# Optimization experiments

Measured on AMD Instinct MI355X. Metric: run time of the kernel, lower is better.

## Reference

```python
import jax, jax.numpy as jnp
import numpy as np

B, C, H, I = 32, 8, 512, 512


def act(x):
    # CustomActivation == hardtanh: (|x+1| - |x-1|) / 2
    return (jnp.abs(x + 1.0) - jnp.abs(x - 1.0)) * 0.5


def setup_inputs() -> dict:
    key = jax.random.key(0)
    ks = jax.random.split(key, 12)
    inp = jax.random.normal(ks[0], (B, C, H, I), dtype=jnp.float32)
    p_mask = jax.random.normal(ks[1], (H, I), dtype=jnp.float32)
    # Wp: tril(randn) with diagonal filled to 1 (matches __init__ + the no_grad
    # tril/clamp projection in forward, which is a no-op right after init).
    Wp = jnp.tril(jax.random.normal(ks[2], (H, H), dtype=jnp.float32))
    Wp = Wp - jnp.diag(jnp.diag(Wp)) + jnp.eye(H, dtype=jnp.float32)
    Wp_diag = jnp.ones((H,), dtype=jnp.float32)
    Wzp = jax.random.normal(ks[3], (H, H), dtype=jnp.float32)
    s = 1.0 / np.sqrt(I)
    def lin(k):
        kw, kb = jax.random.split(k)
        W = jax.random.uniform(kw, (I, I), jnp.float32, -s, s)
        b = jax.random.uniform(kb, (I,), jnp.float32, -s, s)
        return W, b
    p_lin_w, p_lin_b = lin(ks[4])
    z_lin_w, z_lin_b = lin(ks[5])
    fc1_w, fc1_b = lin(ks[6])
    fc2_w, fc2_b = lin(ks[7])
    return {
        'input': inp, 'p_mask': p_mask, 'Wp': Wp, 'Wp_diag': Wp_diag, 'Wzp': Wzp,
        'p_lin_w': p_lin_w, 'p_lin_b': p_lin_b,
        'z_lin_w': z_lin_w, 'z_lin_b': z_lin_b,
        'fc1_w': fc1_w, 'fc1_b': fc1_b, 'fc2_w': fc2_w, 'fc2_b': fc2_b,
    }


def reference(input, p_mask, Wp, Wp_diag, Wzp,
              p_lin_w, p_lin_b, z_lin_w, z_lin_b,
              fc1_w, fc1_b, fc2_w, fc2_b):
    x = input * (1.0 / 5000.0)                      # [B,C,H,I]
    p_set = x * act(p_mask)                         # split_input, broadcast over B,C
    Wp_eff = Wp + jnp.diag(Wp_diag)                 # [H,H]
    # per-channel Wp @ p_set[c], batched over B and C in one GEMM
    tp = jnp.einsum('hk,bcki->bchi', Wp_eff, p_set)
    tp = act(act(tp) @ p_lin_w.T + p_lin_b)         # p_output_layer
    tz = jnp.einsum('hk,bchi->bchi', Wzp, tp)       # wait-free channel-batched GEMM
    tz = act(act(tz) @ z_lin_w.T + z_lin_b)         # z_output_layer
    # sum over in_channel (out_channel==1 so broadcast-accumulate == sum)
    combined = tp.sum(axis=1) + tz.sum(axis=1) + x[:, 0]  # [B,H,I]
    out = jax.nn.relu(combined @ fc1_w.T + fc1_b)
    out = out @ fc2_w.T + fc2_b
    return out
```

## Files before the change

kernel.cpp:

```cpp
#include <hip/hip_runtime.h>

namespace {

constexpr int Bn = 32, Cn = 8, Hn = 512, In = 512;
constexpr size_t HI = (size_t)Hn * In;
constexpr float SC = 1.0f / 5000.0f;

using s16x8 = __attribute__((ext_vector_type(8))) short;
using f32x4 = __attribute__((ext_vector_type(4))) float;

__device__ __forceinline__ float actf(float x) {
    return fminf(1.0f, fmaxf(-1.0f, x));
}

__device__ __forceinline__ unsigned short f2bf(float f) {
    unsigned u = __builtin_bit_cast(unsigned, f);
    u += 0x7FFFu + ((u >> 16) & 1u);
    return (unsigned short)(u >> 16);
}
__device__ __forceinline__ float bf2f(unsigned short h) {
    return __builtin_bit_cast(float, (unsigned)h << 16);
}

__device__ __forceinline__ void async16(const void* g, void* l) {
    __builtin_amdgcn_global_load_lds(
        (const __attribute__((address_space(1))) unsigned*)g,
        (__attribute__((address_space(3))) unsigned*)l, 16, 0, 0);
}

#define CFENCE asm volatile("" ::: "memory")

template<int EPI, bool PCOL, bool TRI>
__global__ __launch_bounds__(256, 3) void mfma_gemm(
    const unsigned short* __restrict__ A,
    const unsigned short* __restrict__ Bt,
    const float* __restrict__ bias,
    const float* __restrict__ zrow,
    unsigned short* __restrict__ out0,
    unsigned short* __restrict__ out1,
    float* __restrict__ outf,
    size_t sB, size_t sC)
{
    __shared__ __align__(16) char lds[2][16384];

    const int tid  = threadIdx.x;
    const int wid  = tid >> 6, lane = tid & 63;
    const int wr   = wid >> 1, wc = wid & 1;
    const int l15  = lane & 15, kq = lane >> 4;

    const int bid = blockIdx.x;
    const int p = ((bid >> 5) << 3) | (bid & 7);
    const int q = (bid >> 3) & 3;
    const int rt = PCOL ? q : p;
    const int ct = PCOL ? (p & 3) : q;
    const size_t zb = PCOL ? (size_t)(p >> 2) : 0;

    const char* Ab = (const char*)A + (size_t)rt * 131072;
    const char* Bb = (const char*)(Bt + zb * sB) + (size_t)ct * 131072;

    f32x4 acc[4][4] = {};

    const int o0  = tid * 16;
    const int r0s = o0 >> 6;
    const int c0s = o0 & 63;
    const int csw = c0s ^ (((r0s >> 1) & 3) << 4);

    auto stage = [&](char* buf, int k0b) {
        async16(Ab + (size_t)r0s * 1024 + k0b + csw,        buf + wid * 1024);
        async16(Ab + (size_t)(64 + r0s) * 1024 + k0b + csw, buf + 4096 + wid * 1024);
        async16(Bb + (size_t)r0s * 1024 + k0b + csw,        buf + 8192 + wid * 1024);
        async16(Bb + (size_t)(64 + r0s) * 1024 + k0b + csw, buf + 12288 + wid * 1024);
    };
    auto compute = [&](const char* buf) {
        s16x8 a[4], b[4];
        const int kx = kq * 16 ^ (((l15 >> 1) & 3) << 4);
        const int ar = wr * 64 + l15;
        const int br = wc * 64 + l15;
        #pragma unroll
        for (int m = 0; m < 4; ++m)
            a[m] = *(const s16x8*)(buf + (size_t)(ar + m * 16) * 64 + kx);
        #pragma unroll
        for (int n = 0; n < 4; ++n)
            b[n] = *(const s16x8*)(buf + 8192 + (size_t)(br + n * 16) * 64 + kx);
        #pragma unroll
        for (int m = 0; m < 4; ++m)
            #pragma unroll
            for (int n = 0; n < 4; ++n)
                acc[m][n] = __builtin_amdgcn_mfma_f32_16x16x32_bf16(a[m], b[n], acc[m][n], 0, 0, 0);
    };

    const int kSteps = TRI ? (rt + 1) * 4 : 16;

    stage(lds[0], 0);
    stage(lds[1], 64);

    #pragma unroll 1
    for (int ks = 0; ks < kSteps; ks += 2) {
        const bool more = (ks + 2 < kSteps);
        asm volatile("s_waitcnt vmcnt(4)" ::: "memory");
        __builtin_amdgcn_s_barrier(); CFENCE;
        compute(lds[0]);
        CFENCE; __builtin_amdgcn_s_barrier();
        if (more) stage(lds[0], (ks + 2) * 64);
        if (more) asm volatile("s_waitcnt vmcnt(4)" ::: "memory");
        else      asm volatile("s_waitcnt vmcnt(0)" ::: "memory");
        __builtin_amdgcn_s_barrier(); CFENCE;
        compute(lds[1]);
        CFENCE; __builtin_amdgcn_s_barrier();
        if (more) stage(lds[1], (ks + 3) * 64);
    }

    const int cb = ct * 128 + wc * 64 + l15;
    const int rb = rt * 128 + wr * 64 + (kq << 2);
    #pragma unroll
    for (int m = 0; m < 4; ++m) {
        #pragma unroll
        for (int n = 0; n < 4; ++n) {
            const int c = cb + n * 16;
            #pragma unroll
            for (int j = 0; j < 4; ++j) {
                const int r = rb + m * 16 + j;
                float v = acc[m][n][j];
                const size_t idx = zb * sC + (size_t)r * 512 + c;
                if (EPI == 0) {
                    out0[idx] = f2bf(actf(v));
                } else if (EPI == 1) {
                    float tp = actf(v + bias[c]);
                    out0[idx] = f2bf(tp);
                    out1[idx] = f2bf(actf(zrow[r & 511] * tp));
                } else if (EPI == 2) {
                    out0[idx] = f2bf(actf(v + bias[c]));
                } else if (EPI == 3) {
                    out0[idx] = f2bf(fmaxf(v + bias[c], 0.0f));
                } else {
                    outf[idx] = v + bias[c];
                }
            }
        }
    }
}

__global__ __launch_bounds__(256) void reduce_both(
    const unsigned short* __restrict__ tp,
    const unsigned short* __restrict__ tz,
    const float* __restrict__ x0,
    unsigned short* __restrict__ comb)
{
    size_t idx = (size_t)blockIdx.x * 256 + threadIdx.x;
    size_t b = idx >> 16;
    size_t p = (idx & 65535) * 4;
    float4 xv = *(const float4*)&x0[(b * Cn) * HI + p];
    float s0 = xv.x * SC, s1 = xv.y * SC, s2 = xv.z * SC, s3 = xv.w * SC;
    #pragma unroll
    for (int c = 0; c < Cn; ++c) {
        size_t q = (b * Cn + c) * HI + p;
        ushort4 a = *(const ushort4*)&tp[q];
        ushort4 d = *(const ushort4*)&tz[q];
        s0 += bf2f(a.x) + bf2f(d.x);
        s1 += bf2f(a.y) + bf2f(d.y);
        s2 += bf2f(a.z) + bf2f(d.z);
        s3 += bf2f(a.w) + bf2f(d.w);
    }
    ushort4 o;
    o.x = f2bf(s0); o.y = f2bf(s1); o.z = f2bf(s2); o.w = f2bf(s3);
    *(ushort4*)&comb[b * HI + p] = o;
}

__global__ __launch_bounds__(256) void transpose_mask(
    const float* __restrict__ x, const float* __restrict__ mask,
    unsigned short* __restrict__ xst)
{
    __shared__ float t[64][65];
    const int bc = blockIdx.z;
    const int i0 = blockIdx.x * 64, k0 = blockIdx.y * 64;
    const int r4 = threadIdx.x >> 6, cc = threadIdx.x & 63;
    const float* xp = x + (size_t)bc * HI;
    #pragma unroll
    for (int it = 0; it < 16; ++it) {
        int kl = it * 4 + r4;
        size_t g = (size_t)(k0 + kl) * In + i0 + cc;
        t[kl][cc] = xp[g] * (actf(mask[g]) * SC);
    }
    __syncthreads();
    unsigned short* op = xst + (size_t)bc * HI;
    #pragma unroll
    for (int it = 0; it < 16; ++it) {
        int il = it * 4 + r4;
        op[(size_t)(i0 + il) * Hn + k0 + cc] = f2bf(t[cc][il]);
    }
}

__global__ __launch_bounds__(256) void prep_wpe_bf(
    const float* __restrict__ Wp, const float* __restrict__ Wpd,
    unsigned short* __restrict__ o)
{
    int idx = blockIdx.x * 256 + threadIdx.x;
    int i = idx >> 9, j = idx & 511;
    o[idx] = f2bf(Wp[idx] + (i == j ? Wpd[i] : 0.0f));
}

__global__ __launch_bounds__(256) void conv_bf(
    const float* __restrict__ s, unsigned short* __restrict__ o)
{
    int idx = blockIdx.x * 256 + threadIdx.x;
    o[idx] = f2bf(s[idx]);
}

__global__ __launch_bounds__(64) void rowsum(
    const float* __restrict__ W, float* __restrict__ zr)
{
    int h = blockIdx.x, l = threadIdx.x;
    float s = 0.0f;
    for (int k = l; k < Hn; k += 64) s += W[h * Hn + k];
    #pragma unroll
    for (int off = 32; off; off >>= 1) s += __shfl_down(s, off, 64);
    if (!l) zr[h] = s;
}

}

extern "C" void kernel_launch(void* const* d_in, const int* in_sizes, int n_in,
                              void* d_out, int out_size, void* d_ws, size_t ws_size,
                              hipStream_t stream)
{
    const float* input  = (const float*)d_in[0];
    const float* p_mask = (const float*)d_in[1];
    const float* Wp     = (const float*)d_in[2];
    const float* Wpd    = (const float*)d_in[3];
    const float* Wzp    = (const float*)d_in[4];
    const float* plw    = (const float*)d_in[5];
    const float* plb    = (const float*)d_in[6];
    const float* zlw    = (const float*)d_in[7];
    const float* zlb    = (const float*)d_in[8];
    const float* f1w    = (const float*)d_in[9];
    const float* f1b    = (const float*)d_in[10];
    const float* f2w    = (const float*)d_in[11];
    const float* f2b    = (const float*)d_in[12];

    constexpr size_t WB = 512 * 512 * 2;
    char* w = (char*)d_ws;
    auto alloc = [&](size_t bytes) { char* p = w; w += (bytes + 255) & ~255ull; return p; };

    unsigned short* Wpeb  = (unsigned short*)alloc(WB);
    unsigned short* plwb  = (unsigned short*)alloc(WB);
    unsigned short* zlwb  = (unsigned short*)alloc(WB);
    unsigned short* f1wb  = (unsigned short*)alloc(WB);
    unsigned short* f2wb  = (unsigned short*)alloc(WB);
    float*          zrw   = (float*)alloc(512 * 4);
    unsigned short* combb = (unsigned short*)alloc((size_t)Bn * HI * 2);
    unsigned short* out1  = (unsigned short*)alloc((size_t)Bn * HI * 2);

    size_t fixedB = (size_t)(w - (char*)d_ws);
    int chunk = 32;
    while (chunk > 1 &&
           fixedB + 4ull * (size_t)chunk * Cn * HI * 2 + 4096 > ws_size)
        chunk >>= 1;
    const size_t CB = (size_t)chunk * Cn * HI * 2;
    unsigned short* xst   = (unsigned short*)alloc(CB);
    unsigned short* tpact = (unsigned short*)alloc(CB);
    unsigned short* tpb   = (unsigned short*)alloc(CB);
    unsigned short* tzin  = (unsigned short*)alloc(CB);
    unsigned short* tzb   = xst;

    prep_wpe_bf<<<512 * 512 / 256, 256, 0, stream>>>(Wp, Wpd, Wpeb);
    conv_bf<<<1024, 256, 0, stream>>>(plw, plwb);
    conv_bf<<<1024, 256, 0, stream>>>(zlw, zlwb);
    conv_bf<<<1024, 256, 0, stream>>>(f1w, f1wb);
    conv_bf<<<1024, 256, 0, stream>>>(f2w, f2wb);
    rowsum<<<512, 64, 0, stream>>>(Wzp, zrw);

    for (int b0 = 0; b0 < Bn; b0 += chunk) {
        const int nc = chunk * Cn;
        const float* inp_c = input + (size_t)b0 * Cn * HI;

        transpose_mask<<<dim3(8, 8, nc), 256, 0, stream>>>(inp_c, p_mask, xst);
        mfma_gemm<0, true, true><<<nc * 16, 256, 0, stream>>>(
            Wpeb, xst, nullptr, nullptr, tpact, nullptr, nullptr, HI, HI);
        mfma_gemm<1, false, false><<<nc * 16, 256, 0, stream>>>(
            tpact, plwb, plb, zrw, tpb, tzin, nullptr, 0, 0);
        mfma_gemm<2, false, false><<<nc * 16, 256, 0, stream>>>(
            tzin, zlwb, zlb, nullptr, tzb, nullptr, nullptr, 0, 0);
        reduce_both<<<chunk * 256, 256, 0, stream>>>(
            tpb, tzb, inp_c, combb + (size_t)b0 * HI);
    }

    mfma_gemm<3, false, false><<<512, 256, 0, stream>>>(
        combb, f1wb, f1b, nullptr, out1, nullptr, nullptr, 0, 0);
    mfma_gemm<4, false, false><<<512, 256, 0, stream>>>(
        out1, f2wb, f2b, nullptr, nullptr, nullptr, (float*)d_out, 0, 0);
}
```

Before: 555.9 us.

## Use 256x256 tiled 8-wave GEMM with interleaved prefetch for main chain

```diff
diff --git a/kernel.cpp b/kernel.cpp
--- a/kernel.cpp
+++ b/kernel.cpp
@@ -29,17 +29,167 @@
 }
 
 #define CFENCE asm volatile("" ::: "memory")
+#define BAR do { CFENCE; __builtin_amdgcn_s_barrier(); CFENCE; } while (0)
 
 template<int EPI, bool PCOL, bool TRI>
-__global__ __launch_bounds__(256, 3) void mfma_gemm(
+__global__ __launch_bounds__(512, 2) void gemm256_8p(
     const unsigned short* __restrict__ A,
     const unsigned short* __restrict__ Bt,
     const float* __restrict__ bias,
     const float* __restrict__ zrow,
     unsigned short* __restrict__ out0,
     unsigned short* __restrict__ out1,
-    float* __restrict__ outf,
     size_t sB, size_t sC)
+{
+    __shared__ __align__(16) char lds[131072];
+    char* daA = lds;
+    char* dbA = lds + 32768;
+    char* daB = lds + 65536;
+    char* dbB = lds + 98304;
+
+    const int tid = threadIdx.x;
+    const int lane = tid & 63, l15 = lane & 15, kq = lane >> 4;
+    const int wid = tid >> 6, wm = wid >> 2, wn = wid & 3;
+
+    const int bid = blockIdx.x;
+    int rt, ct; size_t zb;
+    if (PCOL) {
+        const int p = ((bid >> 5) << 3) | (bid & 7);
+        const int q = (bid >> 3) & 3;
+        zb = (size_t)p; rt = q >> 1; ct = q & 1;
+    } else {
+        const int p = ((bid >> 4) << 3) | (bid & 7);
+        const int q = (bid >> 3) & 1;
+        zb = 0; rt = p; ct = q;
+    }
+
+    const char* Ab = (const char*)A + (size_t)rt * 256 * 1024;
+    const char* Bb = (const char*)(Bt + zb * sB) + (size_t)ct * 256 * 1024;
+
+    const int nkt = TRI ? (rt + 1) * 4 : 8;
+    const int nit = nkt >> 1;
+
+    const int srow8 = tid >> 3;
+    const int csw   = ((tid & 7) ^ (srow8 & 7)) << 4;
+
+    auto stageH = [&](const char* src, int kt, int half, char* dstTile) {
+        const char* s = src + ((size_t)half * 128 + srow8) * 1024 + kt * 128 + csw;
+        char* d = dstTile + half * 16384 + tid * 16;
+        async16(s,             d);
+        async16(s + 64 * 1024, d + 8192);
+    };
+
+    const int kx0 = ((kq    ) ^ (l15 & 7)) << 4;
+    const int kx1 = ((kq + 4) ^ (l15 & 7)) << 4;
+
+    auto rdA4 = [&](const char* tile, int mlo, s16x8 a[2][4]) {
+        #pragma unroll
+        for (int i = 0; i < 4; ++i) {
+            const int row = wm * 128 + (mlo + i) * 16 + l15;
+            a[0][i] = *(const s16x8*)(tile + row * 128 + kx0);
+            a[1][i] = *(const s16x8*)(tile + row * 128 + kx1);
+        }
+    };
+    auto rdB2 = [&](const char* tile, int nlo, s16x8 b[2][2]) {
+        #pragma unroll
+        for (int j = 0; j < 2; ++j) {
+            const int row = wn * 64 + (nlo + j) * 16 + l15;
+            b[0][j] = *(const s16x8*)(tile + row * 128 + kx0);
+            b[1][j] = *(const s16x8*)(tile + row * 128 + kx1);
+        }
+    };
+
+    f32x4 acc[8][4] = {};
+
+    auto QMM = [&](s16x8 a[2][4], s16x8 b[2][2], int mlo, int nlo) {
+        __builtin_amdgcn_s_setprio(1);
+        #pragma unroll
+        for (int kk = 0; kk < 2; ++kk)
+            #pragma unroll
+            for (int i = 0; i < 4; ++i)
+                #pragma unroll
+                for (int j = 0; j < 2; ++j)
+                    acc[mlo + i][nlo + j] = __builtin_amdgcn_mfma_f32_16x16x32_bf16(
+                        a[kk][i], b[kk][j], acc[mlo + i][nlo + j], 0, 0, 0);
+        __builtin_amdgcn_s_setprio(0);
+    };
+
+    stageH(Bb, 0, 0, daB); stageH(Bb, 0, 1, daB);
+    stageH(Ab, 0, 0, daA); stageH(Ab, 0, 1, daA);
+    stageH(Bb, 1, 0, dbB); stageH(Bb, 1, 1, dbB);
+    asm volatile("s_waitcnt vmcnt(4)" ::: "memory");
+    BAR;
+
+    #pragma unroll 1
+    for (int t = 0; t < nit; ++t) {
+        const int j = 2 * t;
+        const bool more = (t + 1 < nit);
+        s16x8 a03[2][4], a47[2][4], b01[2][2], b23[2][2];
+
+        rdA4(daA, 0, a03); rdB2(daB, 0, b01);
+        stageH(Ab, j + 1, 0, dbA);
+        BAR; QMM(a03, b01, 0, 0); BAR;
+        rdB2(daB, 2, b23);
+        stageH(Ab, j + 1, 1, dbA);
+        BAR; QMM(a03, b23, 0, 2); BAR;
+        rdA4(daA, 4, a47);
+        if (more) stageH(Bb, j + 2, 0, daB);
+        BAR; QMM(a47, b23, 4, 2); BAR;
+        if (more) stageH(Bb, j + 2, 1, daB);
+        BAR; QMM(a47, b01, 4, 0);
+        if (more) asm volatile("s_waitcnt vmcnt(4)" ::: "memory");
+        else      asm volatile("s_waitcnt vmcnt(0)" ::: "memory");
+        BAR;
+
+        rdA4(dbA, 0, a03); rdB2(dbB, 0, b01);
+        if (more) stageH(Ab, j + 2, 0, daA);
+        BAR; QMM(a03, b01, 0, 0); BAR;
+        rdB2(dbB, 2, b23);
+        if (more) stageH(Ab, j + 2, 1, daA);
+        BAR; QMM(a03, b23, 0, 2); BAR;
+        rdA4(dbA, 4, a47);
+        if (more) stageH(Bb, j + 3, 0, dbB);
+        BAR; QMM(a47, b23, 4, 2); BAR;
+        if (more) stageH(Bb, j + 3, 1, dbB);
+        BAR; QMM(a47, b01, 4, 0);
+        if (more) { asm volatile("s_waitcnt vmcnt(4)" ::: "memory"); BAR; }
+        else BAR;
+    }
+
+    const int rbase = rt * 256 + wm * 128 + kq * 4;
+    const int cb    = ct * 256 + wn * 64 + l15;
+    #pragma unroll
+    for (int mi = 0; mi < 8; ++mi) {
+        #pragma unroll
+        for (int n = 0; n < 4; ++n) {
+            const int c = cb + n * 16;
+            const float bs = (EPI == 0) ? 0.0f : bias[c];
+            #pragma unroll
+            for (int jj = 0; jj < 4; ++jj) {
+                const size_t r = (size_t)rbase + mi * 16 + jj;
+                const size_t idx = zb * sC + r * 512 + c;
+                float v = acc[mi][n][jj];
+                if (EPI == 0) {
+                    out0[idx] = f2bf(actf(v));
+                } else if (EPI == 1) {
+                    float tp = actf(v + bs);
+                    out0[idx] = f2bf(tp);
+                    out1[idx] = f2bf(actf(zrow[r & 511] * tp));
+                } else {
+                    out0[idx] = f2bf(actf(v + bs));
+                }
+            }
+        }
+    }
+}
+
+template<int EPI>
+__global__ __launch_bounds__(256, 3) void mfma_gemm128(
+    const unsigned short* __restrict__ A,
+    const unsigned short* __restrict__ Bt,
+    const float* __restrict__ bias,
+    unsigned short* __restrict__ out0,
+    float* __restrict__ outf)
 {
     __shared__ __align__(16) char lds[2][16384];
 
@@ -51,12 +201,10 @@
     const int bid = blockIdx.x;
     const int p = ((bid >> 5) << 3) | (bid & 7);
     const int q = (bid >> 3) & 3;
-    const int rt = PCOL ? q : p;
-    const int ct = PCOL ? (p & 3) : q;
-    const size_t zb = PCOL ? (size_t)(p >> 2) : 0;
+    const int rt = p, ct = q;
 
     const char* Ab = (const char*)A + (size_t)rt * 131072;
-    const char* Bb = (const char*)(Bt + zb * sB) + (size_t)ct * 131072;
+    const char* Bb = (const char*)Bt + (size_t)ct * 131072;
 
     f32x4 acc[4][4] = {};
 
@@ -89,55 +237,41 @@
                 acc[m][n] = __builtin_amdgcn_mfma_f32_16x16x32_bf16(a[m], b[n], acc[m][n], 0, 0, 0);
     };
 
-    const int kSteps = TRI ? (rt + 1) * 4 : 16;
-
     stage(lds[0], 0);
     stage(lds[1], 64);
 
     #pragma unroll 1
-    for (int ks = 0; ks < kSteps; ks += 2) {
-        const bool more = (ks + 2 < kSteps);
+    for (int ks = 0; ks < 16; ks += 2) {
+        const bool more = (ks + 2 < 16);
         asm volatile("s_waitcnt vmcnt(4)" ::: "memory");
-        __builtin_amdgcn_s_barrier(); CFENCE;
+        BAR;
         compute(lds[0]);
-        CFENCE; __builtin_amdgcn_s_barrier();
+        BAR;
         if (more) stage(lds[0], (ks + 2) * 64);
         if (more) asm volatile("s_waitcnt vmcnt(4)" ::: "memory");
         else      asm volatile("s_waitcnt vmcnt(0)" ::: "memory");
-        __builtin_amdgcn_s_barrier(); CFENCE;
+        BAR;
         compute(lds[1]);
-        CFENCE; __builtin_amdgcn_s_barrier();
+        BAR;
         if (more) stage(lds[1], (ks + 3) * 64);
     }
 
     const int cb = ct * 128 + wc * 64 + l15;
     const int rb = rt * 128 + wr * 64 + (kq << 2);
     #pragma unroll
-    for (int m = 0; m < 4; ++m) {
+    for (int m = 0; m < 4; ++m)
         #pragma unroll
         for (int n = 0; n < 4; ++n) {
             const int c = cb + n * 16;
             #pragma unroll
             for (int j = 0; j < 4; ++j) {
                 const int r = rb + m * 16 + j;
-                float v = acc[m][n][j];
-                const size_t idx = zb * sC + (size_t)r * 512 + c;
-                if (EPI == 0) {
-                    out0[idx] = f2bf(actf(v));
-                } else if (EPI == 1) {
-                    float tp = actf(v + bias[c]);
-                    out0[idx] = f2bf(tp);
-                    out1[idx] = f2bf(actf(zrow[r & 511] * tp));
-                } else if (EPI == 2) {
-                    out0[idx] = f2bf(actf(v + bias[c]));
-                } else if (EPI == 3) {
-                    out0[idx] = f2bf(fmaxf(v + bias[c], 0.0f));
-                } else {
-                    outf[idx] = v + bias[c];
-                }
+                const size_t idx = (size_t)r * 512 + c;
+                float v = acc[m][n][j] + bias[c];
+                if (EPI == 3) out0[idx] = f2bf(fmaxf(v, 0.0f));
+                else          outf[idx] = v;
             }
         }
-    }
 }
 
 __global__ __launch_bounds__(256) void reduce_both(
@@ -274,18 +408,16 @@
         const float* inp_c = input + (size_t)b0 * Cn * HI;
 
         transpose_mask<<<dim3(8, 8, nc), 256, 0, stream>>>(inp_c, p_mask, xst);
-        mfma_gemm<0, true, true><<<nc * 16, 256, 0, stream>>>(
-            Wpeb, xst, nullptr, nullptr, tpact, nullptr, nullptr, HI, HI);
-        mfma_gemm<1, false, false><<<nc * 16, 256, 0, stream>>>(
-            tpact, plwb, plb, zrw, tpb, tzin, nullptr, 0, 0);
-        mfma_gemm<2, false, false><<<nc * 16, 256, 0, stream>>>(
-            tzin, zlwb, zlb, nullptr, tzb, nullptr, nullptr, 0, 0);
+        gemm256_8p<0, true, true><<<nc * 4, 512, 0, stream>>>(
+            Wpeb, xst, nullptr, nullptr, tpact, nullptr, HI, HI);
+        gemm256_8p<1, false, false><<<nc * 4, 512, 0, stream>>>(
+            tpact, plwb, plb, zrw, tpb, tzin, 0, 0);
+        gemm256_8p<2, false, false><<<nc * 4, 512, 0, stream>>>(
+            tzin, zlwb, zlb, nullptr, tzb, nullptr, 0, 0);
         reduce_both<<<chunk * 256, 256, 0, stream>>>(
             tpb, tzb, inp_c, combb + (size_t)b0 * HI);
     }
 
-    mfma_gemm<3, false, false><<<512, 256, 0, stream>>>(
-        combb, f1wb, f1b, nullptr, out1, nullptr, nullptr, 0, 0);
-    mfma_gemm<4, false, false><<<512, 256, 0, stream>>>(
-        out1, f2wb, f2b, nullptr, nullptr, nullptr, (float*)d_out, 0, 0);
-}
+    mfma_gemm128<3><<<512, 256, 0, stream>>>(combb, f1wb, f1b, out1, nullptr);
+    mfma_gemm128<4><<<512, 256, 0, stream>>>(out1, f2wb, f2b, nullptr, (float*)d_out);
+}
```

Result: faster. 489.5 us (-11.9%).
